# Kernel optimization log

Measured on AMD Instinct MI355X. Metric: run time of the kernel, lower is better.

## Reference

```python
import jax, jax.numpy as jnp
import numpy as np

B, Z, HW = 8, 64, 512          # sparse grid: batch, z-planes, y, x
N_IN = 2_000_000               # active input sites
CIN, COUT = 32, 64
KVOL = 4                       # nplanes*kernel*kernel = 1*2*2
EPS = 1e-4                     # scn BatchNormalization default eps


def _build_rulebook(seed=0):
    """Build gather/scatter rulebook for a [1,2,2] kernel with stride [1,2,2].
    Non-overlapping windows: each input site feeds exactly one (output, offset)."""
    rng = np.random.default_rng(seed)
    b = rng.integers(0, B, N_IN)
    z = rng.integers(0, Z, N_IN)
    y = rng.integers(0, HW, N_IN)
    x = rng.integers(0, HW, N_IN)
    y2, x2 = y // 2, x // 2
    koff = (y % 2) * 2 + (x % 2)                       # kernel offset index in [0,4)
    key_arr = ((b * Z + z) * (HW // 2) + y2) * (HW // 2) + x2
    uniq, out_idx = np.unique(key_arr, return_inverse=True)
    n_out = int(len(uniq))
    P = int(np.bincount(koff, minlength=KVOL).max())   # pad per-offset pair lists
    gidx = np.zeros((KVOL, P), np.int32)               # pad gathers with row 0
    sidx = np.full((KVOL, P), n_out, np.int32)         # pad scatters to dummy row n_out
    for k in range(KVOL):
        sel = np.nonzero(koff == k)[0]
        gidx[k, :len(sel)] = sel
        sidx[k, :len(sel)] = out_idx[sel]
    return gidx, sidx, n_out


def setup_inputs() -> dict:
    key = jax.random.key(0)
    k1, k2, k3, k4 = jax.random.split(key, 4)
    gidx, sidx, n_out = _build_rulebook()
    feats = jax.random.normal(k1, (N_IN, CIN), jnp.float32)
    W = jax.random.normal(k2, (KVOL, CIN, COUT), jnp.float32) * 0.05
    gamma = jax.random.uniform(k3, (COUT,), jnp.float32, 0.5, 1.5)
    beta = jax.random.normal(k4, (COUT,), jnp.float32) * 0.1
    return {"feats": feats, "W": W, "gamma": gamma, "beta": beta,
            "gather_idx": jnp.asarray(gidx), "scatter_idx": jnp.asarray(sidx),
            "n_out": n_out}


def reference(feats, W, gamma, beta, gather_idx, scatter_idx, n_out):
    cout = W.shape[2]
    out = jnp.zeros((n_out + 1, cout), feats.dtype)    # +1 dummy row for padded pairs
    for k in range(W.shape[0]):                        # fixed KVOL=4 kernel offsets
        contrib = feats[gather_idx[k]] @ W[k]          # gather -> GEMM [P,Cout]
        out = out.at[scatter_idx[k]].add(contrib)      # scatter-accumulate
    out = out[:n_out]
    # BatchNorm over active sites (training-mode batch stats, biased variance)
    mean = out.mean(axis=0)
    var = out.var(axis=0)
    out = (out - mean) * jax.lax.rsqrt(var + EPS) * gamma + beta
    return jax.nn.relu(out)
```

## Files before the change

### kernel.cpp

```cpp
#include <hip/hip_runtime.h>

#define EPS_LN 1e-4f

typedef short short8 __attribute__((ext_vector_type(8)));
typedef float f32x4 __attribute__((ext_vector_type(4)));

__device__ __forceinline__ short f2bf(float f) {
  const unsigned u = __float_as_uint(f);
  return (short)((u + 0x7FFFu + ((u >> 16) & 1u)) >> 16);
}


__global__ __launch_bounds__(256) void flag_kernel(
    const int* __restrict__ sidx, unsigned* __restrict__ flags, int P,
    int n_out) {
  const int k = blockIdx.y;
  const int p = blockIdx.x * blockDim.x + threadIdx.x;
  if (p >= P) return;
  const int s = sidx[k * P + p];
  if (s >= n_out) return;
  const unsigned sh = (s & 15) << 1;
  const unsigned old = atomicOr(&flags[s >> 4], 1u << sh);
  if (old & (1u << sh)) atomicOr(&flags[s >> 4], 2u << sh);
}

__global__ __launch_bounds__(256) void zero_multi_kernel(
    const unsigned* __restrict__ flags, float4* __restrict__ out, int nwords,
    int n_out) {
  const int stride = gridDim.x * blockDim.x;
  const float4 z = {0.f, 0.f, 0.f, 0.f};
  for (int w = blockIdx.x * blockDim.x + threadIdx.x; w < nwords; w += stride) {
    unsigned f = flags[w] & 0xAAAAAAAAu;
    while (f) {
      const int b = __builtin_ctz(f);
      f &= f - 1;
      const int r = (w << 4) + (b >> 1);
      if (r < n_out) {
        float4* row = out + ((size_t)r << 4);
#pragma unroll
        for (int j = 0; j < 16; ++j) row[j] = z;
      }
    }
  }
}

__global__ __launch_bounds__(256) void conv_mfma_kernel(
    const float* __restrict__ feats, const float* __restrict__ W,
    const int* __restrict__ gidx, const int* __restrict__ sidx,
    const unsigned* __restrict__ flags, float* __restrict__ out,
    float* __restrict__ ws, int P, int n_out, int rpw) {
  const int lane = threadIdx.x & 63;
  const int l15 = lane & 15;
  const int lh = lane >> 4;
  const int k = blockIdx.y;
  const int wv = blockIdx.x * (blockDim.x >> 6) + (threadIdx.x >> 6);

  __shared__ float ls[128];
  if (threadIdx.x < 128) ls[threadIdx.x] = 0.f;
  __syncthreads();

  short8 wb[4];
#pragma unroll
  for (int m = 0; m < 4; ++m) {
#pragma unroll
    for (int j = 0; j < 8; ++j) {
      const int kk = (lh << 3) + j;
      wb[m][j] = f2bf(W[(((k << 5) + kk) << 6) + (m << 4) + l15]);
    }
  }

  const long base = (long)k * P;
  const int start = wv * rpw;
  const int end = min(start + rpw, P);
  float s1[4] = {0.f, 0.f, 0.f, 0.f}, s2[4] = {0.f, 0.f, 0.f, 0.f};
  const f32x4 zero = {0.f, 0.f, 0.f, 0.f};

  if (start < end) {
    int g = 0, sp = (n_out << 1);
    {
      const int pg = start + lane;
      if (pg < end) {
        g = gidx[base + pg];
        const int s = sidx[base + pg];
        const unsigned mu = (flags[s >> 4] >> (((s & 15) << 1) + 1)) & 1u;
        sp = (s << 1) | (int)mu;
      }
    }

    for (int gs = start; gs < end; gs += 64) {
      float4 F[8];
#pragma unroll
      for (int t = 0; t < 4; ++t) {
        const int gq = __shfl(g, (t << 4) + l15);
        const float4* fp = (const float4*)feats + ((size_t)gq << 3) + (lh << 1);
        F[2 * t] = fp[0];
        F[2 * t + 1] = fp[1];
      }
      int gN = 0, spN = (n_out << 1);
      {
        const int pg = gs + 64 + lane;
        if (pg < end) {
          gN = gidx[base + pg];
          const int s = sidx[base + pg];
          const unsigned mu = (flags[s >> 4] >> (((s & 15) << 1) + 1)) & 1u;
          spN = (s << 1) | (int)mu;
        }
      }
#pragma unroll
      for (int t = 0; t < 4; ++t) {
        short8 a;
#pragma unroll
        for (int j = 0; j < 4; ++j) {
          a[j] = f2bf(((const float*)&F[2 * t])[j]);
          a[4 + j] = f2bf(((const float*)&F[2 * t + 1])[j]);
        }
        const f32x4 d0 = __builtin_amdgcn_mfma_f32_16x16x32_bf16(a, wb[0], zero, 0, 0, 0);
        const f32x4 d1 = __builtin_amdgcn_mfma_f32_16x16x32_bf16(a, wb[1], zero, 0, 0, 0);
        const f32x4 d2 = __builtin_amdgcn_mfma_f32_16x16x32_bf16(a, wb[2], zero, 0, 0, 0);
        const f32x4 d3 = __builtin_amdgcn_mfma_f32_16x16x32_bf16(a, wb[3], zero, 0, 0, 0);
#pragma unroll
        for (int q = 0; q < 4; ++q) {
          const int spq = __shfl(sp, (t << 4) + (lh << 2) + q);
          const int srow = spq >> 1;
          const bool mu = (spq & 1) != 0;
          const bool v = srow < n_out;
          const size_t rb = ((size_t)srow << 6) + l15;
#define DO_STORE(dm, m)                                                 \
          {                                                             \
            const float val = dm[q];                                    \
            if (v) {                                                    \
              s1[m] += val;                                             \
              if (mu) {                                                 \
                const float old = atomicAdd(out + rb + (m << 4), val);  \
                s2[m] = fmaf(val, 2.f * old + val, s2[m]);              \
              } else {                                                  \
                out[rb + (m << 4)] = val;                               \
                s2[m] = fmaf(val, val, s2[m]);                          \
              }                                                         \
            }                                                           \
          }
          DO_STORE(d0, 0)
          DO_STORE(d1, 1)
          DO_STORE(d2, 2)
          DO_STORE(d3, 3)
#undef DO_STORE
        }
      }
      g = gN;
      sp = spN;
    }
  }

#pragma unroll
  for (int m = 0; m < 4; ++m) {
    atomicAdd(&ls[(m << 4) + l15], s1[m]);
    atomicAdd(&ls[64 + (m << 4) + l15], s2[m]);
  }
  __syncthreads();
  if (threadIdx.x < 128) atomicAdd(&ws[threadIdx.x], ls[threadIdx.x]);
}

__global__ void finalize_stats_kernel(float* __restrict__ ws,
                                      const float* __restrict__ gamma,
                                      const float* __restrict__ beta,
                                      float inv_n) {
  const int c = threadIdx.x;
  const float mean = ws[c] * inv_n;
  const float var = ws[64 + c] * inv_n - mean * mean;
  const float sc = rsqrtf(var + EPS_LN) * gamma[c];
  ws[128 + c] = sc;
  ws[192 + c] = beta[c] - mean * sc;
}

__global__ __launch_bounds__(256) void normalize_kernel(
    float4* __restrict__ out, const float* __restrict__ ws, long total4) {
  const long stride = (long)gridDim.x * blockDim.x;
  const int cb = (threadIdx.x << 2) & 63;
  const float4 sc = *(const float4*)(ws + 128 + cb);
  const float4 sh = *(const float4*)(ws + 192 + cb);
  for (long i = (long)blockIdx.x * blockDim.x + threadIdx.x; i < total4; i += stride) {
    float4 x = out[i];
    x.x = fmaxf(fmaf(x.x, sc.x, sh.x), 0.f);
    x.y = fmaxf(fmaf(x.y, sc.y, sh.y), 0.f);
    x.z = fmaxf(fmaf(x.z, sc.z, sh.z), 0.f);
    x.w = fmaxf(fmaf(x.w, sc.w, sh.w), 0.f);
    out[i] = x;
  }
}

__global__ __launch_bounds__(256) void scatter_conv_kernel(
    const float* __restrict__ feats, const float* __restrict__ W,
    const int* __restrict__ gidx, const int* __restrict__ sidx,
    float* __restrict__ out, int P, int n_out) {
  const int lane = threadIdx.x & 63;
  const int k = blockIdx.y;
  const int wave = blockIdx.x * (blockDim.x >> 6) + (threadIdx.x >> 6);
  const int stride = gridDim.x * (blockDim.x >> 6);
  float w[32];
#pragma unroll
  for (int c = 0; c < 32; ++c) w[c] = W[((k * 32 + c) << 6) + lane];
  const int base = k * P;
  for (int p = wave; p < P; p += stride) {
    const int g = gidx[base + p];
    const int s = sidx[base + p];
    const float4* fp = (const float4*)(feats + (long)g * 32);
    float4 f[8];
#pragma unroll
    for (int j = 0; j < 8; ++j) f[j] = fp[j];
    float a0 = 0, a1 = 0, a2 = 0, a3 = 0;
#pragma unroll
    for (int j = 0; j < 8; ++j) {
      a0 = fmaf(f[j].x, w[4 * j + 0], a0);
      a1 = fmaf(f[j].y, w[4 * j + 1], a1);
      a2 = fmaf(f[j].z, w[4 * j + 2], a2);
      a3 = fmaf(f[j].w, w[4 * j + 3], a3);
    }
    if (s < n_out) atomicAdd(out + ((long)s << 6) + lane, (a0 + a1) + (a2 + a3));
  }
}

__global__ __launch_bounds__(256) void stats_kernel(
    const float4* __restrict__ out, float* __restrict__ ws, long total4) {
  const long stride = (long)gridDim.x * blockDim.x;
  float s1[4] = {0.f, 0.f, 0.f, 0.f};
  float s2[4] = {0.f, 0.f, 0.f, 0.f};
  for (long i = (long)blockIdx.x * blockDim.x + threadIdx.x; i < total4; i += stride) {
    float4 x = out[i];
    s1[0] += x.x; s2[0] += x.x * x.x;
    s1[1] += x.y; s2[1] += x.y * x.y;
    s1[2] += x.z; s2[2] += x.z * x.z;
    s1[3] += x.w; s2[3] += x.w * x.w;
  }
  __shared__ float ls[128];
  if (threadIdx.x < 128) ls[threadIdx.x] = 0.f;
  __syncthreads();
  const int cb = (threadIdx.x << 2) & 63;
#pragma unroll
  for (int j = 0; j < 4; ++j) {
    atomicAdd(&ls[cb + j], s1[j]);
    atomicAdd(&ls[64 + cb + j], s2[j]);
  }
  __syncthreads();
  if (threadIdx.x < 128) atomicAdd(&ws[threadIdx.x], ls[threadIdx.x]);
}

extern "C" void kernel_launch(void* const* d_in, const int* in_sizes, int n_in,
                              void* d_out, int out_size, void* d_ws, size_t ws_size,
                              hipStream_t stream) {
  const float* feats = (const float*)d_in[0];
  const float* W     = (const float*)d_in[1];
  const float* gamma = (const float*)d_in[2];
  const float* beta  = (const float*)d_in[3];
  const int*   gidx  = (const int*)d_in[4];
  const int*   sidx  = (const int*)d_in[5];

  const int P = in_sizes[4] / 4;
  const int n_out = out_size / 64;
  float* out = (float*)d_out;
  float* ws  = (float*)d_ws;
  const long total4 = (long)out_size / 4;

  char* wsb = (char*)d_ws;
  const size_t flags_off = 2048;
  const int nwords = (n_out + 16) / 16 + 1;
  const size_t flags_bytes = (size_t)nwords * 4;
  const size_t need = flags_off + flags_bytes;

  if (ws_size >= need) {
    unsigned* flags = (unsigned*)(wsb + flags_off);
    hipMemsetAsync(wsb, 0, 2048, stream);
    hipMemsetAsync(flags, 0, flags_bytes, stream);

    dim3 fgrid((P + 255) / 256, 4);
    flag_kernel<<<fgrid, 256, 0, stream>>>(sidx, flags, P, n_out);
    zero_multi_kernel<<<1024, 256, 0, stream>>>(flags, (float4*)out, nwords, n_out);

    const int rpw = 256;
    const int waves_per_k = (P + rpw - 1) / rpw;
    dim3 vgrid((waves_per_k + 3) / 4, 4);
    conv_mfma_kernel<<<vgrid, 256, 0, stream>>>(feats, W, gidx, sidx, flags,
                                                out, ws, P, n_out, rpw);
    finalize_stats_kernel<<<1, 64, 0, stream>>>(ws, gamma, beta, 1.0f / (float)n_out);
    normalize_kernel<<<2048, 256, 0, stream>>>((float4*)out, ws, total4);
  } else {
    hipMemsetAsync(d_out, 0, (size_t)out_size * sizeof(float), stream);
    hipMemsetAsync(d_ws, 0, 256 * sizeof(float), stream);
    dim3 sgrid(2048, 4);
    scatter_conv_kernel<<<sgrid, 256, 0, stream>>>(feats, W, gidx, sidx, out, P, n_out);
    stats_kernel<<<2048, 256, 0, stream>>>((const float4*)out, ws, total4);
    finalize_stats_kernel<<<1, 64, 0, stream>>>(ws, gamma, beta, 1.0f / (float)n_out);
    normalize_kernel<<<2048, 256, 0, stream>>>((float4*)out, ws, total4);
  }
}
```

Measured before the change: 541.2 us.

## Double-buffer feature gathers to overlap loads with MFMA compute and stores

Restructures the conv main loop into a two-stage software pipeline with two register buffers of gathered feature rows. The next 64-pair chunk's gather is issued before the current chunk's MFMA and scatter work, and index loads run two chunks ahead. The aim is to hide gather latency behind compute and stores, at the cost of more live registers (an extra 8 float4 plus indices), which may lower occupancy.

```diff
diff --git a/kernel.cpp b/kernel.cpp
--- a/kernel.cpp
+++ b/kernel.cpp
@@ -44,6 +44,78 @@
   }
 }
 
+
+__device__ __forceinline__ void load_idx(
+    const int* __restrict__ gidx, const int* __restrict__ sidx,
+    const unsigned* __restrict__ flags, long base, int pg, int end_,
+    int n_out, int& g, int& sp) {
+  g = 0;
+  sp = (n_out << 1);
+  if (pg < end_) {
+    g = gidx[base + pg];
+    const int s = sidx[base + pg];
+    const unsigned mu = (flags[s >> 4] >> (((s & 15) << 1) + 1)) & 1u;
+    sp = (s << 1) | (int)mu;
+  }
+}
+
+__device__ __forceinline__ void gather8(const float* __restrict__ feats,
+                                        int g, int l15, int lh, float4* F) {
+#pragma unroll
+  for (int t = 0; t < 4; ++t) {
+    const int gq = __shfl(g, (t << 4) + l15);
+    const float4* fp = (const float4*)feats + ((size_t)gq << 3) + (lh << 1);
+    F[2 * t] = fp[0];
+    F[2 * t + 1] = fp[1];
+  }
+}
+
+__device__ __forceinline__ void compute_store(
+    const float4* F, int sp, const short8* wb, int l15, int lh,
+    float* __restrict__ out, int n_out, float* s1, float* s2) {
+  const f32x4 zero = {0.f, 0.f, 0.f, 0.f};
+#pragma unroll
+  for (int t = 0; t < 4; ++t) {
+    short8 a;
+#pragma unroll
+    for (int j = 0; j < 4; ++j) {
+      a[j] = f2bf(((const float*)&F[2 * t])[j]);
+      a[4 + j] = f2bf(((const float*)&F[2 * t + 1])[j]);
+    }
+    const f32x4 d0 = __builtin_amdgcn_mfma_f32_16x16x32_bf16(a, wb[0], zero, 0, 0, 0);
+    const f32x4 d1 = __builtin_amdgcn_mfma_f32_16x16x32_bf16(a, wb[1], zero, 0, 0, 0);
+    const f32x4 d2 = __builtin_amdgcn_mfma_f32_16x16x32_bf16(a, wb[2], zero, 0, 0, 0);
+    const f32x4 d3 = __builtin_amdgcn_mfma_f32_16x16x32_bf16(a, wb[3], zero, 0, 0, 0);
+#pragma unroll
+    for (int q = 0; q < 4; ++q) {
+      const int spq = __shfl(sp, (t << 4) + (lh << 2) + q);
+      const int srow = spq >> 1;
+      const bool mu = (spq & 1) != 0;
+      const bool v = srow < n_out;
+      const size_t rb = ((size_t)srow << 6) + l15;
+#define DO_STORE(dm, m)                                             \
+      {                                                             \
+        const float val = dm[q];                                    \
+        if (v) {                                                    \
+          s1[m] += val;                                             \
+          if (mu) {                                                 \
+            const float old = atomicAdd(out + rb + (m << 4), val);  \
+            s2[m] = fmaf(val, 2.f * old + val, s2[m]);              \
+          } else {                                                  \
+            out[rb + (m << 4)] = val;                               \
+            s2[m] = fmaf(val, val, s2[m]);                          \
+          }                                                         \
+        }                                                           \
+      }
+      DO_STORE(d0, 0)
+      DO_STORE(d1, 1)
+      DO_STORE(d2, 2)
+      DO_STORE(d3, 3)
+#undef DO_STORE
+    }
+  }
+}
+
 __global__ __launch_bounds__(256) void conv_mfma_kernel(
     const float* __restrict__ feats, const float* __restrict__ W,
     const int* __restrict__ gidx, const int* __restrict__ sidx,
@@ -73,81 +145,25 @@
   const int start = wv * rpw;
   const int end = min(start + rpw, P);
   float s1[4] = {0.f, 0.f, 0.f, 0.f}, s2[4] = {0.f, 0.f, 0.f, 0.f};
-  const f32x4 zero = {0.f, 0.f, 0.f, 0.f};
 
   if (start < end) {
-    int g = 0, sp = (n_out << 1);
-    {
-      const int pg = start + lane;
-      if (pg < end) {
-        g = gidx[base + pg];
-        const int s = sidx[base + pg];
-        const unsigned mu = (flags[s >> 4] >> (((s & 15) << 1) + 1)) & 1u;
-        sp = (s << 1) | (int)mu;
-      }
-    }
-
-    for (int gs = start; gs < end; gs += 64) {
-      float4 F[8];
-#pragma unroll
-      for (int t = 0; t < 4; ++t) {
-        const int gq = __shfl(g, (t << 4) + l15);
-        const float4* fp = (const float4*)feats + ((size_t)gq << 3) + (lh << 1);
-        F[2 * t] = fp[0];
-        F[2 * t + 1] = fp[1];
-      }
-      int gN = 0, spN = (n_out << 1);
-      {
-        const int pg = gs + 64 + lane;
-        if (pg < end) {
-          gN = gidx[base + pg];
-          const int s = sidx[base + pg];
-          const unsigned mu = (flags[s >> 4] >> (((s & 15) << 1) + 1)) & 1u;
-          spN = (s << 1) | (int)mu;
-        }
-      }
-#pragma unroll
-      for (int t = 0; t < 4; ++t) {
-        short8 a;
-#pragma unroll
-        for (int j = 0; j < 4; ++j) {
-          a[j] = f2bf(((const float*)&F[2 * t])[j]);
-          a[4 + j] = f2bf(((const float*)&F[2 * t + 1])[j]);
-        }
-        const f32x4 d0 = __builtin_amdgcn_mfma_f32_16x16x32_bf16(a, wb[0], zero, 0, 0, 0);
-        const f32x4 d1 = __builtin_amdgcn_mfma_f32_16x16x32_bf16(a, wb[1], zero, 0, 0, 0);
-        const f32x4 d2 = __builtin_amdgcn_mfma_f32_16x16x32_bf16(a, wb[2], zero, 0, 0, 0);
-        const f32x4 d3 = __builtin_amdgcn_mfma_f32_16x16x32_bf16(a, wb[3], zero, 0, 0, 0);
-#pragma unroll
-        for (int q = 0; q < 4; ++q) {
-          const int spq = __shfl(sp, (t << 4) + (lh << 2) + q);
-          const int srow = spq >> 1;
-          const bool mu = (spq & 1) != 0;
-          const bool v = srow < n_out;
-          const size_t rb = ((size_t)srow << 6) + l15;
-#define DO_STORE(dm, m)                                                 \
-          {                                                             \
-            const float val = dm[q];                                    \
-            if (v) {                                                    \
-              s1[m] += val;                                             \
-              if (mu) {                                                 \
-                const float old = atomicAdd(out + rb + (m << 4), val);  \
-                s2[m] = fmaf(val, 2.f * old + val, s2[m]);              \
-              } else {                                                  \
-                out[rb + (m << 4)] = val;                               \
-                s2[m] = fmaf(val, val, s2[m]);                          \
-              }                                                         \
-            }                                                           \
-          }
-          DO_STORE(d0, 0)
-          DO_STORE(d1, 1)
-          DO_STORE(d2, 2)
-          DO_STORE(d3, 3)
-#undef DO_STORE
-        }
-      }
-      g = gN;
-      sp = spN;
+    int gA, spA, gB, spB, gC, spC, gD, spD;
+    float4 FA[8], FB[8];
+
+    load_idx(gidx, sidx, flags, base, start + lane, end, n_out, gA, spA);
+    gather8(feats, gA, l15, lh, FA);
+    load_idx(gidx, sidx, flags, base, start + 64 + lane, end, n_out, gB, spB);
+
+    for (int gs = start; gs < end; gs += 128) {
+      const bool hasB = (gs + 64 < end);
+      if (hasB) gather8(feats, gB, l15, lh, FB);
+      load_idx(gidx, sidx, flags, base, gs + 128 + lane, end, n_out, gC, spC);
+      compute_store(FA, spA, wb, l15, lh, out, n_out, s1, s2);
+      if (gs + 128 < end) gather8(feats, gC, l15, lh, FA);
+      load_idx(gidx, sidx, flags, base, gs + 192 + lane, end, n_out, gD, spD);
+      if (hasB) compute_store(FB, spB, wb, l15, lh, out, n_out, s1, s2);
+      gA = gC; spA = spC;
+      gB = gD; spB = spD;
     }
   }
 
```

Result: slower. 566.8 us (+4.7%).

## Stage single-contributor conv outputs as bf16 in workspace and normalize per row

Applied to the files above, without the earlier changes.

Rows hit by only one input site now have their conv result written as packed bf16 into a workspace buffer instead of fp32 to the output. Multi-contributor rows still use fp32 atomics into the output. A new row-wise normalize kernel picks each row's source from the flags, then applies batchnorm and ReLU into the output. The bf16 conversion also moves to the packed hardware instruction. This halves intermediate write traffic for most rows but rounds those values to bf16 before normalization, costs an extra flag read per row, and requires a larger workspace, falling back to the slow path if it is too small.

```diff
diff --git a/kernel.cpp b/kernel.cpp
--- a/kernel.cpp
+++ b/kernel.cpp
@@ -8,6 +8,12 @@
 __device__ __forceinline__ short f2bf(float f) {
   const unsigned u = __float_as_uint(f);
   return (short)((u + 0x7FFFu + ((u >> 16) & 1u)) >> 16);
+}
+
+__device__ __forceinline__ unsigned cvt_pk_bf16(float a, float b) {
+  unsigned r;
+  asm("v_cvt_pk_bf16_f32 %0, %1, %2" : "=v"(r) : "v"(a), "v"(b));
+  return r;
 }
 
 
@@ -48,7 +54,8 @@
     const float* __restrict__ feats, const float* __restrict__ W,
     const int* __restrict__ gidx, const int* __restrict__ sidx,
     const unsigned* __restrict__ flags, float* __restrict__ out,
-    float* __restrict__ ws, int P, int n_out, int rpw) {
+    unsigned short* __restrict__ wsbuf, float* __restrict__ ws,
+    int P, int n_out, int rpw) {
   const int lane = threadIdx.x & 63;
   const int l15 = lane & 15;
   const int lh = lane >> 4;
@@ -108,12 +115,13 @@
       }
 #pragma unroll
       for (int t = 0; t < 4; ++t) {
+        unsigned au0 = cvt_pk_bf16(F[2 * t].x, F[2 * t].y);
+        unsigned au1 = cvt_pk_bf16(F[2 * t].z, F[2 * t].w);
+        unsigned au2 = cvt_pk_bf16(F[2 * t + 1].x, F[2 * t + 1].y);
+        unsigned au3 = cvt_pk_bf16(F[2 * t + 1].z, F[2 * t + 1].w);
         short8 a;
-#pragma unroll
-        for (int j = 0; j < 4; ++j) {
-          a[j] = f2bf(((const float*)&F[2 * t])[j]);
-          a[4 + j] = f2bf(((const float*)&F[2 * t + 1])[j]);
-        }
+        ((unsigned*)&a)[0] = au0; ((unsigned*)&a)[1] = au1;
+        ((unsigned*)&a)[2] = au2; ((unsigned*)&a)[3] = au3;
         const f32x4 d0 = __builtin_amdgcn_mfma_f32_16x16x32_bf16(a, wb[0], zero, 0, 0, 0);
         const f32x4 d1 = __builtin_amdgcn_mfma_f32_16x16x32_bf16(a, wb[1], zero, 0, 0, 0);
         const f32x4 d2 = __builtin_amdgcn_mfma_f32_16x16x32_bf16(a, wb[2], zero, 0, 0, 0);
@@ -122,28 +130,30 @@
         for (int q = 0; q < 4; ++q) {
           const int spq = __shfl(sp, (t << 4) + (lh << 2) + q);
           const int srow = spq >> 1;
-          const bool mu = (spq & 1) != 0;
-          const bool v = srow < n_out;
-          const size_t rb = ((size_t)srow << 6) + l15;
-#define DO_STORE(dm, m)                                                 \
-          {                                                             \
-            const float val = dm[q];                                    \
-            if (v) {                                                    \
-              s1[m] += val;                                             \
-              if (mu) {                                                 \
-                const float old = atomicAdd(out + rb + (m << 4), val);  \
-                s2[m] = fmaf(val, 2.f * old + val, s2[m]);              \
-              } else {                                                  \
-                out[rb + (m << 4)] = val;                               \
-                s2[m] = fmaf(val, val, s2[m]);                          \
-              }                                                         \
-            }                                                           \
+          if (srow < n_out) {
+            const float v0 = d0[q], v1 = d1[q], v2 = d2[q], v3 = d3[q];
+            s1[0] += v0; s1[1] += v1; s1[2] += v2; s1[3] += v3;
+            if (spq & 1) {
+              const size_t rb = ((size_t)srow << 6) + l15;
+              const float o0 = atomicAdd(out + rb, v0);
+              const float o1 = atomicAdd(out + rb + 16, v1);
+              const float o2 = atomicAdd(out + rb + 32, v2);
+              const float o3 = atomicAdd(out + rb + 48, v3);
+              s2[0] = fmaf(v0, 2.f * o0 + v0, s2[0]);
+              s2[1] = fmaf(v1, 2.f * o1 + v1, s2[1]);
+              s2[2] = fmaf(v2, 2.f * o2 + v2, s2[2]);
+              s2[3] = fmaf(v3, 2.f * o3 + v3, s2[3]);
+            } else {
+              s2[0] = fmaf(v0, v0, s2[0]);
+              s2[1] = fmaf(v1, v1, s2[1]);
+              s2[2] = fmaf(v2, v2, s2[2]);
+              s2[3] = fmaf(v3, v3, s2[3]);
+              uint2 pk;
+              pk.x = cvt_pk_bf16(v0, v1);
+              pk.y = cvt_pk_bf16(v2, v3);
+              *(uint2*)(wsbuf + ((size_t)srow << 6) + (l15 << 2)) = pk;
+            }
           }
-          DO_STORE(d0, 0)
-          DO_STORE(d1, 1)
-          DO_STORE(d2, 2)
-          DO_STORE(d3, 3)
-#undef DO_STORE
         }
       }
       g = gN;
@@ -170,6 +180,89 @@
   const float sc = rsqrtf(var + EPS_LN) * gamma[c];
   ws[128 + c] = sc;
   ws[192 + c] = beta[c] - mean * sc;
+}
+
+__global__ __launch_bounds__(256) void normalize_rows_kernel(
+    const unsigned short* __restrict__ wsbuf, const unsigned* __restrict__ flags,
+    const float* __restrict__ ws, float* __restrict__ out, int n_out) {
+  const int lane = threadIdx.x & 63;
+  const float sc = ws[128 + lane];
+  const float sh = ws[192 + lane];
+  const int poff = ((lane & 15) << 2) + (lane >> 4);
+  const int wave = (blockIdx.x * blockDim.x + threadIdx.x) >> 6;
+  const int wstep = (gridDim.x * blockDim.x) >> 6;
+
+  for (int r = wave * 2; r < n_out; r += wstep * 2) {
+    const int r1 = r + 1;
+    const bool has1 = r1 < n_out;
+    const bool mu0 = (flags[r >> 4] >> (((r & 15) << 1) + 1)) & 1u;
+    const bool mu1 = has1 ? ((flags[r1 >> 4] >> (((r1 & 15) << 1) + 1)) & 1u) : false;
+    float v0, v1 = 0.f;
+    if (mu0) v0 = out[((size_t)r << 6) + lane];
+    else v0 = __uint_as_float((unsigned)wsbuf[((size_t)r << 6) + poff] << 16);
+    if (has1) {
+      if (mu1) v1 = out[((size_t)r1 << 6) + lane];
+      else v1 = __uint_as_float((unsigned)wsbuf[((size_t)r1 << 6) + poff] << 16);
+    }
+    out[((size_t)r << 6) + lane] = fmaxf(fmaf(v0, sc, sh), 0.f);
+    if (has1) out[((size_t)r1 << 6) + lane] = fmaxf(fmaf(v1, sc, sh), 0.f);
+  }
+}
+
+__global__ __launch_bounds__(256) void scatter_conv_kernel(
+    const float* __restrict__ feats, const float* __restrict__ W,
+    const int* __restrict__ gidx, const int* __restrict__ sidx,
+    float* __restrict__ out, int P, int n_out) {
+  const int lane = threadIdx.x & 63;
+  const int k = blockIdx.y;
+  const int wave = blockIdx.x * (blockDim.x >> 6) + (threadIdx.x >> 6);
+  const int stride = gridDim.x * (blockDim.x >> 6);
+  float w[32];
+#pragma unroll
+  for (int c = 0; c < 32; ++c) w[c] = W[((k * 32 + c) << 6) + lane];
+  const int base = k * P;
+  for (int p = wave; p < P; p += stride) {
+    const int g = gidx[base + p];
+    const int s = sidx[base + p];
+    const float4* fp = (const float4*)(feats + (long)g * 32);
+    float4 f[8];
+#pragma unroll
+    for (int j = 0; j < 8; ++j) f[j] = fp[j];
+    float a0 = 0, a1 = 0, a2 = 0, a3 = 0;
+#pragma unroll
+    for (int j = 0; j < 8; ++j) {
+      a0 = fmaf(f[j].x, w[4 * j + 0], a0);
+      a1 = fmaf(f[j].y, w[4 * j + 1], a1);
+      a2 = fmaf(f[j].z, w[4 * j + 2], a2);
+      a3 = fmaf(f[j].w, w[4 * j + 3], a3);
+    }
+    if (s < n_out) atomicAdd(out + ((long)s << 6) + lane, (a0 + a1) + (a2 + a3));
+  }
+}
+
+__global__ __launch_bounds__(256) void stats_kernel(
+    const float4* __restrict__ out, float* __restrict__ ws, long total4) {
+  const long stride = (long)gridDim.x * blockDim.x;
+  float s1[4] = {0.f, 0.f, 0.f, 0.f};
+  float s2[4] = {0.f, 0.f, 0.f, 0.f};
+  for (long i = (long)blockIdx.x * blockDim.x + threadIdx.x; i < total4; i += stride) {
+    float4 x = out[i];
+    s1[0] += x.x; s2[0] += x.x * x.x;
+    s1[1] += x.y; s2[1] += x.y * x.y;
+    s1[2] += x.z; s2[2] += x.z * x.z;
+    s1[3] += x.w; s2[3] += x.w * x.w;
+  }
+  __shared__ float ls[128];
+  if (threadIdx.x < 128) ls[threadIdx.x] = 0.f;
+  __syncthreads();
+  const int cb = (threadIdx.x << 2) & 63;
+#pragma unroll
+  for (int j = 0; j < 4; ++j) {
+    atomicAdd(&ls[cb + j], s1[j]);
+    atomicAdd(&ls[64 + cb + j], s2[j]);
+  }
+  __syncthreads();
+  if (threadIdx.x < 128) atomicAdd(&ws[threadIdx.x], ls[threadIdx.x]);
 }
 
 __global__ __launch_bounds__(256) void normalize_kernel(
@@ -188,62 +281,6 @@
   }
 }
 
-__global__ __launch_bounds__(256) void scatter_conv_kernel(
-    const float* __restrict__ feats, const float* __restrict__ W,
-    const int* __restrict__ gidx, const int* __restrict__ sidx,
-    float* __restrict__ out, int P, int n_out) {
-  const int lane = threadIdx.x & 63;
-  const int k = blockIdx.y;
-  const int wave = blockIdx.x * (blockDim.x >> 6) + (threadIdx.x >> 6);
-  const int stride = gridDim.x * (blockDim.x >> 6);
-  float w[32];
-#pragma unroll
-  for (int c = 0; c < 32; ++c) w[c] = W[((k * 32 + c) << 6) + lane];
-  const int base = k * P;
-  for (int p = wave; p < P; p += stride) {
-    const int g = gidx[base + p];
-    const int s = sidx[base + p];
-    const float4* fp = (const float4*)(feats + (long)g * 32);
-    float4 f[8];
-#pragma unroll
-    for (int j = 0; j < 8; ++j) f[j] = fp[j];
-    float a0 = 0, a1 = 0, a2 = 0, a3 = 0;
-#pragma unroll
-    for (int j = 0; j < 8; ++j) {
-      a0 = fmaf(f[j].x, w[4 * j + 0], a0);
-      a1 = fmaf(f[j].y, w[4 * j + 1], a1);
-      a2 = fmaf(f[j].z, w[4 * j + 2], a2);
-      a3 = fmaf(f[j].w, w[4 * j + 3], a3);
-    }
-    if (s < n_out) atomicAdd(out + ((long)s << 6) + lane, (a0 + a1) + (a2 + a3));
-  }
-}
-
-__global__ __launch_bounds__(256) void stats_kernel(
-    const float4* __restrict__ out, float* __restrict__ ws, long total4) {
-  const long stride = (long)gridDim.x * blockDim.x;
-  float s1[4] = {0.f, 0.f, 0.f, 0.f};
-  float s2[4] = {0.f, 0.f, 0.f, 0.f};
-  for (long i = (long)blockIdx.x * blockDim.x + threadIdx.x; i < total4; i += stride) {
-    float4 x = out[i];
-    s1[0] += x.x; s2[0] += x.x * x.x;
-    s1[1] += x.y; s2[1] += x.y * x.y;
-    s1[2] += x.z; s2[2] += x.z * x.z;
-    s1[3] += x.w; s2[3] += x.w * x.w;
-  }
-  __shared__ float ls[128];
-  if (threadIdx.x < 128) ls[threadIdx.x] = 0.f;
-  __syncthreads();
-  const int cb = (threadIdx.x << 2) & 63;
-#pragma unroll
-  for (int j = 0; j < 4; ++j) {
-    atomicAdd(&ls[cb + j], s1[j]);
-    atomicAdd(&ls[64 + cb + j], s2[j]);
-  }
-  __syncthreads();
-  if (threadIdx.x < 128) atomicAdd(&ws[threadIdx.x], ls[threadIdx.x]);
-}
-
 extern "C" void kernel_launch(void* const* d_in, const int* in_sizes, int n_in,
                               void* d_out, int out_size, void* d_ws, size_t ws_size,
                               hipStream_t stream) {
@@ -264,10 +301,12 @@
   const size_t flags_off = 2048;
   const int nwords = (n_out + 16) / 16 + 1;
   const size_t flags_bytes = (size_t)nwords * 4;
-  const size_t need = flags_off + flags_bytes;
+  const size_t buf_off = (flags_off + flags_bytes + 255) & ~(size_t)255;
+  const size_t need = buf_off + (size_t)n_out * 128;
 
   if (ws_size >= need) {
     unsigned* flags = (unsigned*)(wsb + flags_off);
+    unsigned short* wsbuf = (unsigned short*)(wsb + buf_off);
     hipMemsetAsync(wsb, 0, 2048, stream);
     hipMemsetAsync(flags, 0, flags_bytes, stream);
 
@@ -279,9 +318,9 @@
     const int waves_per_k = (P + rpw - 1) / rpw;
     dim3 vgrid((waves_per_k + 3) / 4, 4);
     conv_mfma_kernel<<<vgrid, 256, 0, stream>>>(feats, W, gidx, sidx, flags,
-                                                out, ws, P, n_out, rpw);
+                                                out, wsbuf, ws, P, n_out, rpw);
     finalize_stats_kernel<<<1, 64, 0, stream>>>(ws, gamma, beta, 1.0f / (float)n_out);
-    normalize_kernel<<<2048, 256, 0, stream>>>((float4*)out, ws, total4);
+    normalize_rows_kernel<<<2048, 256, 0, stream>>>(wsbuf, flags, ws, out, n_out);
   } else {
     hipMemsetAsync(d_out, 0, (size_t)out_size * sizeof(float), stream);
     hipMemsetAsync(d_ws, 0, 256 * sizeof(float), stream);
```

Measured after the change: 525.3 us. -2.9%, faster.
